# Optimization experiments

Measured on AMD Instinct MI355X. Metric: run time of the kernel, lower is better.

The kernel has to match this reference:

```python
import jax, jax.numpy as jnp
import numpy as np

B, P, H, E, A, V, L = 64, 196, 512, 512, 512, 30000, 21  # batch, pixels, hidden, embed, attn, vocab, cap_len
T = L - 1  # max decode steps


def setup_inputs() -> dict:
    key = jax.random.key(0)
    ks = jax.random.split(key, 16)
    s = 0.02
    lengths = jnp.sort(jax.random.randint(ks[2], (B,), 5, L + 1))[::-1]
    lengths = lengths.at[0].set(L)  # ensure max decode length == T
    return {
        "encoder_out": jax.random.normal(ks[0], (B, P, H), jnp.float32),
        "captions": jax.random.randint(ks[1], (B, L), 0, V),
        "lengths": lengths,
        "emb": jax.random.normal(ks[3], (V, E), jnp.float32) * s,
        "W_ea": jax.random.normal(ks[4], (A, H), jnp.float32) * s,
        "b_ea": jnp.zeros((A,), jnp.float32),
        "W_da": jax.random.normal(ks[5], (A, H), jnp.float32) * s,
        "b_da": jnp.zeros((A,), jnp.float32),
        "W_fa": jax.random.normal(ks[6], (1, A), jnp.float32) * s,
        "b_fa": jnp.zeros((1,), jnp.float32),
        "W_fb": jax.random.normal(ks[7], (H, H), jnp.float32) * s,
        "b_fb": jnp.zeros((H,), jnp.float32),
        "W_ih": jax.random.normal(ks[8], (4 * H, E + H), jnp.float32) * s,
        "W_hh": jax.random.normal(ks[9], (4 * H, H), jnp.float32) * s,
        "b_ih": jnp.zeros((4 * H,), jnp.float32),
        "b_hh": jnp.zeros((4 * H,), jnp.float32),
        "W_fc": jax.random.normal(ks[10], (V, H), jnp.float32) * s,
        "b_fc": jnp.zeros((V,), jnp.float32),
    }


def reference(encoder_out, captions, lengths, emb, W_ea, b_ea, W_da, b_da,
              W_fa, b_fa, W_fb, b_fb, W_ih, W_hh, b_ih, b_hh, W_fc, b_fc):
    # init hidden state = mean over pixels
    h0 = encoder_out.mean(axis=1)  # (B, H)
    c0 = h0
    # precompute encoder attention projection (loop-invariant)
    att1 = jnp.einsum("bph,ah->bpa", encoder_out, W_ea) + b_ea  # (B, P, A)
    emb_seq = emb[captions[:, :T]]  # (B, T, E)
    # active[t, b] = decode_length_b > t  (captions assumed sorted desc by length)
    active = (lengths[None, :] - 1) > jnp.arange(T)[:, None]  # (T, B)

    def step(carry, xs):
        h, c = carry
        emb_t, act = xs  # (B, E), (B,)
        # Bahdanau attention
        att2 = h @ W_da.T + b_da  # (B, A)
        e = (jax.nn.relu(att1 + att2[:, None, :]) @ W_fa.T).squeeze(-1) + b_fa[0]  # (B, P)
        alpha = jax.nn.softmax(e, axis=1)
        awe = jnp.einsum("bph,bp->bh", encoder_out, alpha)  # (B, H)
        gate = jax.nn.sigmoid(h @ W_fb.T + b_fb)
        awe = gate * awe
        x = jnp.concatenate([emb_t, awe], axis=1)  # (B, E+H)
        gates = x @ W_ih.T + b_ih + h @ W_hh.T + b_hh  # (B, 4H)
        i, f, g, o = jnp.split(gates, 4, axis=1)
        c_new = jax.nn.sigmoid(f) * c + jax.nn.sigmoid(i) * jnp.tanh(g)
        h_new = jax.nn.sigmoid(o) * jnp.tanh(c_new)
        preds = h_new @ W_fc.T + b_fc  # (B, V)
        m = act[:, None].astype(h.dtype)
        return (h_new, c_new), (preds * m, alpha * m)

    (_, _), (preds_t, alphas_t) = jax.lax.scan(
        step, (h0, c0), (emb_seq.transpose(1, 0, 2), active))
    predictions = preds_t.transpose(1, 0, 2)  # (B, T, V)
    alphas = alphas_t.transpose(1, 0, 2)      # (B, T, P)
    return predictions, alphas
```

## Files before the change

### kernel.cpp

```cpp
#include <hip/hip_runtime.h>
#include <hip/hip_bf16.h>

typedef _Float16 f16;
typedef __attribute__((ext_vector_type(8))) _Float16 f16x8;
typedef __attribute__((ext_vector_type(2))) _Float16 f16x2;
typedef __attribute__((ext_vector_type(4))) float f32x4;

constexpr int CB = 64, CP = 196, CH = 512, CV = 30000, CVP = 30080, CT = 20;
constexpr int NT = 235;

__device__ __forceinline__ float sigf(float x) { return 1.f / (1.f + __expf(-x)); }

#if defined(__has_builtin)
#if __has_builtin(__builtin_amdgcn_fdot2)
#define HAVE_FDOT2 1
#endif
#endif

__device__ __forceinline__ f16x2 asf16x2(unsigned u) {
    union { unsigned x; f16x2 h; } c; c.x = u; return c.h;
}
__device__ __forceinline__ float dotp(f16x2 a, f16x2 b, float c) {
#ifdef HAVE_FDOT2
    return __builtin_amdgcn_fdot2(a, b, c, false);
#else
    return fmaf((float)a[0], (float)b[0], fmaf((float)a[1], (float)b[1], c));
#endif
}

__device__ __forceinline__ unsigned ald_u(const unsigned* p) {
    return __hip_atomic_load(p, __ATOMIC_RELAXED, __HIP_MEMORY_SCOPE_AGENT);
}
__device__ __forceinline__ void ast_u(unsigned* p, unsigned v) {
    __hip_atomic_store(p, v, __ATOMIC_RELAXED, __HIP_MEMORY_SCOPE_AGENT);
}
__device__ __forceinline__ float ald_f(const float* p) {
    return __hip_atomic_load(p, __ATOMIC_RELAXED, __HIP_MEMORY_SCOPE_AGENT);
}
__device__ __forceinline__ void ast_f(float* p, float v) {
    __hip_atomic_store(p, v, __ATOMIC_RELAXED, __HIP_MEMORY_SCOPE_AGENT);
}

__device__ __forceinline__ void wait4(const int* slotbase, int target) {
    if (threadIdx.x < 64) {
        for (;;) {
            int v = __hip_atomic_load(slotbase + (threadIdx.x & 3), __ATOMIC_RELAXED,
                                      __HIP_MEMORY_SCOPE_AGENT);
            if (__all(v >= target)) break;
            __builtin_amdgcn_s_sleep(1);
        }
    }
    __builtin_amdgcn_s_barrier();
    __builtin_amdgcn_sched_barrier(0);
}
__device__ __forceinline__ void post4(int* slot, int val) {
    __syncthreads();
    if (threadIdx.x == 0)
        __hip_atomic_store(slot, val, __ATOMIC_RELAXED, __HIP_MEMORY_SCOPE_AGENT);
}

__device__ __forceinline__ void cvt8(const float* __restrict__ s, f16* __restrict__ d) {
    float4 a = *(const float4*)s;
    float4 b = *(const float4*)(s + 4);
    f16x8 o;
    o[0] = (f16)a.x; o[1] = (f16)a.y; o[2] = (f16)a.z; o[3] = (f16)a.w;
    o[4] = (f16)b.x; o[5] = (f16)b.y; o[6] = (f16)b.z; o[7] = (f16)b.w;
    *(f16x8*)d = o;
}

__global__ __launch_bounds__(256) void k_mega(
    const float* __restrict__ enc, const float* __restrict__ W_ea,
    const float* __restrict__ W_da, const float* __restrict__ W_fb,
    const float* __restrict__ W_ih, const float* __restrict__ W_hh,
    const float* __restrict__ W_fc, const float* __restrict__ emb,
    const int* __restrict__ caps, const float* __restrict__ b_da,
    const float* __restrict__ b_fb, const float* __restrict__ b_ih,
    const float* __restrict__ b_hh,
    f16* __restrict__ enc_h, f16* __restrict__ Wea_h, f16* __restrict__ W1q4,
    f16* __restrict__ BpQ4, f16* __restrict__ WihE_p, f16* __restrict__ Wfc_h,
    f16* __restrict__ embg, float* __restrict__ bcat, float* __restrict__ bsum_p,
    int* __restrict__ gsync)
{
    constexpr long long E0 = 802816;
    constexpr long long E1 = E0 + 32768;
    constexpr long long E2 = E1 + 1920000;
    constexpr long long E3 = E2 + 5120;
    constexpr long long E4 = E3 + 81920;
    constexpr long long E5 = E4 + 65536;
    constexpr long long E6 = E5 + 262144;
    constexpr long long E7 = E6 + 131072;
    constexpr long long E8 = E7 + 3072;
    constexpr long long TOT = E8 + 4096;

    for (long long id = (long long)blockIdx.x * 256 + threadIdx.x; id < TOT;
         id += (long long)gridDim.x * 256) {
        if (id < E0) {
            cvt8(enc + id * 8, enc_h + id * 8);
        } else if (id < E1) {
            long long c = id - E0; cvt8(W_ea + c * 8, Wea_h + c * 8);
        } else if (id < E2) {
            long long c = id - E1; cvt8(W_fc + c * 8, Wfc_h + c * 8);
        } else if (id < E3) {
            long long c = id - E2; f16x8 z = {};
            *(f16x8*)&Wfc_h[15360000 + c * 8] = z;
        } else if (id < E4) {
            long long c = id - E3; int m = (int)(c >> 6), j = (int)(c & 63);
            int tt = m >> 6, bb = m & 63;
            int row = caps[bb * 21 + tt];
            cvt8(emb + (size_t)row * 512 + j * 8, embg + (size_t)m * 512 + j * 8);
        } else if (id < E5) {
            long long c = id - E4;
            int qq = (int)(c >> 14), kk4 = (int)((c >> 8) & 63), o = (int)(c & 255);
            const float* src = (o < 128) ? &W_da[(size_t)(128 * qq + o) * 512]
                                         : &W_fb[(size_t)(128 * qq + o - 128) * 512];
            cvt8(src + kk4 * 8, &W1q4[(((size_t)qq * 64 + kk4) * 256 + o) * 8]);
        } else if (id < E6) {
            long long c = id - E5;
            int qq = (int)(c >> 16), kk4 = (int)((c >> 9) & 127), o = (int)(c & 511);
            int d = 128 * qq + (o >> 2), g = o & 3;
            int r = g * 512 + d;
            const float* src = (kk4 < 64) ? &W_ih[(size_t)r * 1024 + 512 + kk4 * 8]
                                          : &W_hh[(size_t)r * 512 + kk4 * 8 - 512];
            cvt8(src, &BpQ4[(((size_t)qq * 128 + kk4) * 512 + o) * 8]);
        } else if (id < E7) {
            long long c = id - E6;
            int cc = (int)(c >> 6), j8 = (int)(c & 63);
            int r = (cc & 3) * 512 + (cc >> 2);
            cvt8(W_ih + (size_t)r * 1024 + j8 * 8, WihE_p + (size_t)cc * 512 + j8 * 8);
        } else if (id < E8) {
            int i = (int)(id - E7);
            if (i < 512) bcat[i] = b_da[i];
            else if (i < 1024) bcat[i] = b_fb[i - 512];
            else {
                int cc = i - 1024;
                int r = (cc & 3) * 512 + (cc >> 2);
                bsum_p[cc] = b_ih[r] + b_hh[r];
            }
        } else {
            gsync[(int)(id - E8)] = 0;
        }
    }
}

__global__ __launch_bounds__(256) void k_h0(const float* __restrict__ enc,
                                            f16* __restrict__ hbuf, float* __restrict__ cinit)
{
    int b = blockIdx.x;
    for (int h = threadIdx.x; h < CH; h += 256) {
        const float* p = enc + (size_t)b * CP * CH + h;
        float s = 0.f;
        for (int q = 0; q < CP; ++q) s += p[q * CH];
        s *= (1.f / 196.f);
        hbuf[b * CH + h] = (f16)s;
        cinit[b * CH + h] = s;
    }
}

enum { EPI_F16B = 0, EPI_F32B = 1, EPI_PREDS = 2 };

template <int EPI>
__global__ __launch_bounds__(256) void gemm_k512(
    const f16* __restrict__ Aptr, const f16* __restrict__ Bptr, int N,
    const float* __restrict__ bias, float* __restrict__ Cf,
    f16* __restrict__ Ch, const int* __restrict__ lengths)
{
    constexpr int LD = 40;
    const int tid = threadIdx.x;
    const int lane = tid & 63, wave = tid >> 6;
    const int wr = wave >> 1, wc = wave & 1;
    int bx, by;
    if constexpr (EPI == EPI_PREDS) {
        int bid1 = blockIdx.x;
        int nt = (bid1 / 80) * 8 + (bid1 & 7);
        int mt = (bid1 >> 3) % 10;
        if (nt >= NT) return;
        bx = nt; by = mt;
    } else {
        bx = blockIdx.x; by = blockIdx.y;
    }

    __shared__ f16 As[128 * LD];
    __shared__ f16 Bs[128 * LD];

    const f16* Ag = Aptr + (size_t)by * 128 * 512;
    const f16* Bg = Bptr + (size_t)bx * 128 * 512;

    int srow[2], skc[2];
#pragma unroll
    for (int i = 0; i < 2; ++i) { int ci = tid + i * 256; srow[i] = ci >> 2; skc[i] = (ci & 3) * 8; }

    f32x4 acc[4][4] = {};
    f16x8 ar[2], br[2];
#pragma unroll
    for (int i = 0; i < 2; ++i) {
        ar[i] = *(const f16x8*)&Ag[(size_t)srow[i] * 512 + skc[i]];
        br[i] = *(const f16x8*)&Bg[(size_t)srow[i] * 512 + skc[i]];
    }

    const int rr = lane & 15, kg = (lane >> 4) * 8;
    for (int kt = 0; kt < 16; ++kt) {
        __syncthreads();
#pragma unroll
        for (int i = 0; i < 2; ++i) {
            *(f16x8*)&As[srow[i] * LD + skc[i]] = ar[i];
            *(f16x8*)&Bs[srow[i] * LD + skc[i]] = br[i];
        }
        __syncthreads();
        if (kt < 15) {
            int k0 = (kt + 1) * 32;
#pragma unroll
            for (int i = 0; i < 2; ++i) {
                ar[i] = *(const f16x8*)&Ag[(size_t)srow[i] * 512 + k0 + skc[i]];
                br[i] = *(const f16x8*)&Bg[(size_t)srow[i] * 512 + k0 + skc[i]];
            }
        }
        f16x8 af[4], bf[4];
#pragma unroll
        for (int mi = 0; mi < 4; ++mi) af[mi] = *(const f16x8*)&As[(wr * 64 + mi * 16 + rr) * LD + kg];
#pragma unroll
        for (int ni = 0; ni < 4; ++ni) bf[ni] = *(const f16x8*)&Bs[(wc * 64 + ni * 16 + rr) * LD + kg];
#pragma unroll
        for (int mi = 0; mi < 4; ++mi)
#pragma unroll
            for (int ni = 0; ni < 4; ++ni)
                acc[mi][ni] = __builtin_amdgcn_mfma_f32_16x16x32_f16(af[mi], bf[ni], acc[mi][ni], 0, 0, 0);
    }

    const int m0 = by * 128 + wr * 64;
    const int n0 = bx * 128 + wc * 64;
    const int r0 = (lane >> 4) * 4, cc = lane & 15;
#pragma unroll
    for (int mi = 0; mi < 4; ++mi) {
#pragma unroll
        for (int ni = 0; ni < 4; ++ni) {
#pragma unroll
            for (int r = 0; r < 4; ++r) {
                int m = m0 + mi * 16 + r0 + r;
                int n = n0 + ni * 16 + cc;
                float v = acc[mi][ni][r];
                if constexpr (EPI == EPI_F16B) {
                    Ch[(size_t)m * N + n] = (f16)(v + bias[n]);
                } else if constexpr (EPI == EPI_F32B) {
                    Cf[(size_t)m * N + n] = v + bias[n];
                } else {
                    if (n < CV) {
                        int tt = m >> 6, b = m & 63;
                        float val = ((lengths[b] - 1) > tt) ? (v + bias[n]) : 0.f;
                        __builtin_nontemporal_store(val, &Cf[(size_t)b * (CT * CV) + (size_t)tt * CV + n]);
                    }
                }
            }
        }
    }
}

__global__ __launch_bounds__(512) void k_loop4(
    const f16* __restrict__ att1, const f16* __restrict__ ench,
    const f16* __restrict__ W1q4, const f16* __restrict__ BpQ4,
    const float* __restrict__ embIH, const float* __restrict__ Wfa,
    const float* __restrict__ bfa, const float* __restrict__ bcat,
    const int* __restrict__ lens, const float* __restrict__ cinit,
    f16* __restrict__ hbuf, float* __restrict__ alph,
    float* __restrict__ xatt2, float* __restrict__ xe,
    float* __restrict__ xxa, int* __restrict__ gsync)
{
    const int bid = blockIdx.x, tid = threadIdx.x;
    const int lane = tid & 63, wv = tid >> 6;
    const int b = bid >> 2, q = bid & 3;

    int* s1 = gsync + b * 16;
    int* s2 = gsync + 1024 + b * 16;
    int* s3 = gsync + 2048 + b * 16;
    int* s4 = gsync + 3072 + b * 16;

    __shared__ __align__(16) f16 h_s[512];
    __shared__ float c_s[128];
    __shared__ float a2f[512];
    __shared__ float ga_s[128];
    __shared__ float es[196], als[196], red[16];
    __shared__ float part1[2][256];
    __shared__ float awp[32][128];
    __shared__ __align__(16) f16 xh_s[1024];
    __shared__ float gt[512];
    __shared__ f16 htmp[128];

    if (tid < 256) ((unsigned*)h_s)[tid] = ((const unsigned*)(hbuf + b * 512))[tid];
    if (tid < 128) c_s[tid] = cinit[b * 512 + 128 * q + tid];
    const float bfa0 = bfa[0];
    const int lb = lens[b];
    float wfr[8];
#pragma unroll
    for (int j = 0; j < 8; ++j) wfr[j] = Wfa[lane * 8 + j];
    const int ecnt = (56 - wv) >> 3;
    const int ar_ = lane >> 4, ac_ = lane & 15;
    __syncthreads();

    for (int t = 0; t < CT; ++t) {
        if (t > 0) {
            wait4(s4, t);
            if (tid < 256)
                ((unsigned*)h_s)[tid] =
                    ald_u((const unsigned*)(hbuf + (size_t)t * 32768 + b * 512) + tid);
            __syncthreads();
        }

        {
            const int kh = tid >> 8, oo = tid & 255;
            const f16* wp = W1q4 + (((size_t)q * 64 + kh * 32) * 256 + oo) * 8;
            const uint4* xq = (const uint4*)h_s + kh * 32;
            float a0 = 0.f, a1 = 0.f, a2 = 0.f, a3 = 0.f;
#pragma unroll 8
            for (int i = 0; i < 32; ++i) {
                uint4 w = *(const uint4*)(wp + (size_t)i * 2048);
                uint4 xv = xq[i];
                a0 = dotp(asf16x2(w.x), asf16x2(xv.x), a0);
                a1 = dotp(asf16x2(w.y), asf16x2(xv.y), a1);
                a2 = dotp(asf16x2(w.z), asf16x2(xv.z), a2);
                a3 = dotp(asf16x2(w.w), asf16x2(xv.w), a3);
            }
            part1[kh][oo] = (a0 + a1) + (a2 + a3);
        }
        __syncthreads();
        if (tid < 256) {
            float v = part1[0][tid] + part1[1][tid];
            if (tid < 128) {
                v += bcat[128 * q + tid];
                ast_f(&xatt2[b * 512 + 128 * q + tid], v);
            } else {
                ga_s[tid - 128] = v + bcat[512 + 128 * q + (tid - 128)];
            }
        }

        f16x8 fr[7];
#pragma unroll
        for (int i = 0; i < 7; ++i)
            if (i < ecnt)
                fr[i] = *(const f16x8*)&att1[((size_t)b * CP + 49 * q + wv + 8 * i) * 512 + lane * 8];

        post4(s1 + q, t + 1);
        wait4(s1, t + 1);
        a2f[tid] = ald_f(&xatt2[b * 512 + tid]);
        __syncthreads();

        {
            float a2r[8];
#pragma unroll
            for (int j = 0; j < 8; ++j) a2r[j] = a2f[lane * 8 + j];
#pragma unroll
            for (int i = 0; i < 7; ++i)
                if (i < ecnt) {
                    float e = 0.f;
#pragma unroll
                    for (int j = 0; j < 8; ++j)
                        e += fmaxf((float)fr[i][j] + a2r[j], 0.f) * wfr[j];
#pragma unroll
                    for (int o = 32; o; o >>= 1) e += __shfl_down(e, o);
                    if (lane == 0) ast_f(&xe[b * 196 + 49 * q + wv + 8 * i], e + bfa0);
                }
        }

        f16x8 er[7];
#pragma unroll
        for (int it = 0; it < 7; ++it) {
            int p = it * 32 + wv * 4 + ar_;
            if (p < CP)
                er[it] = *(const f16x8*)&ench[((size_t)b * CP + p) * 512 + 128 * q + ac_ * 8];
        }

        post4(s2 + q, t + 1);
        wait4(s2, t + 1);
        if (tid < CP) es[tid] = ald_f(&xe[b * 196 + tid]);
        __syncthreads();

        {
            float ev = (tid < CP) ? es[tid] : -1e30f;
            float mx = ev;
#pragma unroll
            for (int o = 32; o; o >>= 1) mx = fmaxf(mx, __shfl_down(mx, o));
            if (lane == 0) red[wv] = mx;
            __syncthreads();
            mx = red[0];
#pragma unroll
            for (int w = 1; w < 8; ++w) mx = fmaxf(mx, red[w]);
            float ex = (tid < CP) ? __expf(ev - mx) : 0.f;
            float sm = ex;
#pragma unroll
            for (int o = 32; o; o >>= 1) sm += __shfl_down(sm, o);
            if (lane == 0) red[8 + wv] = sm;
            __syncthreads();
            sm = red[8];
#pragma unroll
            for (int w = 1; w < 8; ++w) sm += red[8 + w];
            float al = ex / sm;
            if (tid < CP) {
                als[tid] = al;
                if (tid >= 49 * q && tid < 49 * (q + 1))
                    alph[(size_t)b * (CT * CP) + t * CP + tid] = ((lb - 1) > t) ? al : 0.f;
            }
        }
        __syncthreads();
        {
            float aw[8] = {};
#pragma unroll
            for (int it = 0; it < 7; ++it) {
                int p = it * 32 + wv * 4 + ar_;
                if (p < CP) {
                    float a = als[p];
#pragma unroll
                    for (int j = 0; j < 8; ++j) aw[j] = fmaf(a, (float)er[it][j], aw[j]);
                }
            }
#pragma unroll
            for (int j = 0; j < 8; ++j) awp[wv * 4 + ar_][ac_ * 8 + j] = aw[j];
        }
        __syncthreads();
        if (tid < 128) {
            float s = 0.f;
#pragma unroll
            for (int g = 0; g < 32; ++g) s += awp[g][tid];
            ast_f(&xxa[b * 512 + 128 * q + tid], sigf(ga_s[tid]) * s);
        }
        post4(s3 + q, t + 1);
        wait4(s3, t + 1);
        xh_s[tid] = (f16)ald_f(&xxa[b * 512 + tid]);
        xh_s[512 + tid] = h_s[tid];
        __syncthreads();

        {
            const f16* wp = BpQ4 + ((size_t)q * 128 * 512 + tid) * 8;
            const uint4* xq = (const uint4*)xh_s;
            float a0 = 0.f, a1 = 0.f, a2 = 0.f, a3 = 0.f;
#pragma unroll 8
            for (int i = 0; i < 128; ++i) {
                uint4 w = *(const uint4*)(wp + (size_t)i * 4096);
                uint4 xv = xq[i];
                a0 = dotp(asf16x2(w.x), asf16x2(xv.x), a0);
                a1 = dotp(asf16x2(w.y), asf16x2(xv.y), a1);
                a2 = dotp(asf16x2(w.z), asf16x2(xv.z), a2);
                a3 = dotp(asf16x2(w.w), asf16x2(xv.w), a3);
            }
            gt[tid] = (a0 + a1) + (a2 + a3)
                      + embIH[(size_t)(t * 64 + b) * 2048 + 512 * q + tid];
        }
        __syncthreads();
        if (tid < 128) {
            float gi = gt[4 * tid], gf = gt[4 * tid + 1];
            float gg = gt[4 * tid + 2], go = gt[4 * tid + 3];
            float cn = sigf(gf) * c_s[tid] + sigf(gi) * tanhf(gg);
            c_s[tid] = cn;
            htmp[tid] = (f16)(sigf(go) * tanhf(cn));
        }
        __syncthreads();
        if (tid < 64) {
            union { f16 h[2]; unsigned u; } pk;
            pk.h[0] = htmp[2 * tid]; pk.h[1] = htmp[2 * tid + 1];
            ast_u((unsigned*)&hbuf[(size_t)(t + 1) * 32768 + b * 512 + 128 * q] + tid, pk.u);
        }
        post4(s4 + q, t + 1);
    }
}

extern "C" void kernel_launch(void* const* d_in, const int* in_sizes, int n_in,
                              void* d_out, int out_size, void* d_ws, size_t ws_size,
                              hipStream_t stream)
{
    const float* enc  = (const float*)d_in[0];
    const int*   caps = (const int*)d_in[1];
    const int*   lens = (const int*)d_in[2];
    const float* emb  = (const float*)d_in[3];
    const float* W_ea = (const float*)d_in[4];
    const float* b_ea = (const float*)d_in[5];
    const float* W_da = (const float*)d_in[6];
    const float* b_da = (const float*)d_in[7];
    const float* W_fa = (const float*)d_in[8];
    const float* b_fa = (const float*)d_in[9];
    const float* W_fb = (const float*)d_in[10];
    const float* b_fb = (const float*)d_in[11];
    const float* W_ih = (const float*)d_in[12];
    const float* W_hh = (const float*)d_in[13];
    const float* b_ih = (const float*)d_in[14];
    const float* b_hh = (const float*)d_in[15];
    const float* W_fc = (const float*)d_in[16];
    const float* b_fc = (const float*)d_in[17];

    float* out = (float*)d_out;
    float* alph_out = out + (size_t)CB * CT * CV;

    char* p = (char*)d_ws;
    auto carve = [&](size_t bytes) {
        char* r = p;
        p += (bytes + 255) & ~(size_t)255;
        return r;
    };
    f16* enc_h   = (f16*)carve((size_t)12544 * 512 * 2);
    f16* att1_h  = (f16*)carve((size_t)12544 * 512 * 2);
    f16* Wea_h   = (f16*)carve((size_t)512 * 512 * 2);
    f16* W1q4    = (f16*)carve((size_t)4 * 64 * 256 * 8 * 2);
    f16* BpQ4    = (f16*)carve((size_t)4 * 128 * 512 * 8 * 2);
    f16* WihE_p  = (f16*)carve((size_t)2048 * 512 * 2);
    f16* Wfc_h   = (f16*)carve((size_t)CVP * 512 * 2);
    f16* embg    = (f16*)carve((size_t)1280 * 512 * 2);
    float* embIH = (float*)carve((size_t)1280 * 2048 * 4);
    float* bcat  = (float*)carve(1024 * 4);
    float* bsum_p= (float*)carve(2048 * 4);
    f16* hbuf    = (f16*)carve((size_t)21 * 64 * 512 * 2);
    float* cinit = (float*)carve((size_t)64 * 512 * 4);
    float* xatt2 = (float*)carve((size_t)64 * 512 * 4);
    float* xe    = (float*)carve((size_t)64 * 196 * 4);
    float* xxa   = (float*)carve((size_t)64 * 512 * 4);
    int* gsync   = (int*)carve(4096 * 4);

    hipLaunchKernelGGL(k_mega, dim3(4096), dim3(256), 0, stream,
                       enc, W_ea, W_da, W_fb, W_ih, W_hh, W_fc, emb, caps,
                       b_da, b_fb, b_ih, b_hh,
                       enc_h, Wea_h, W1q4, BpQ4, WihE_p, Wfc_h, embg, bcat, bsum_p, gsync);

    hipLaunchKernelGGL(k_h0, dim3(64), dim3(256), 0, stream, enc, hbuf, cinit);

    hipLaunchKernelGGL((gemm_k512<EPI_F16B>), dim3(4, 98), dim3(256), 0, stream,
                       enc_h, Wea_h, 512, b_ea, (float*)nullptr, att1_h, (const int*)nullptr);
    hipLaunchKernelGGL((gemm_k512<EPI_F32B>), dim3(16, 10), dim3(256), 0, stream,
                       embg, WihE_p, 2048, bsum_p, embIH, (f16*)nullptr, (const int*)nullptr);

    hipLaunchKernelGGL(k_loop4, dim3(256), dim3(512), 0, stream,
                       att1_h, enc_h, W1q4, BpQ4, embIH, W_fa, b_fa, bcat,
                       lens, cinit, hbuf, alph_out, xatt2, xe, xxa, gsync);

    hipLaunchKernelGGL((gemm_k512<EPI_PREDS>), dim3(2400), dim3(256), 0, stream,
                       hbuf + 32768, Wfc_h, CVP, b_fc, out, (f16*)nullptr, lens);
}
```

Before: 553.8 us.

## Regroup recurrent loop blocks so each weight slice serves four batch rows

The persistent decode loop is repartitioned from 4 blocks per batch row to groups of 16 blocks sharing 4 batch rows. Each block now owns a slice of the output features for the W_da/W_fb and LSTM gate matvecs and applies it to all 4 rows at once. This cuts the per-step weight traffic from L2 by reusing each loaded weight element across four hidden vectors. In exchange, sync barriers now span 16 blocks instead of 4, and the h/gate data must be exchanged across the wider group through global memory.

New measurement: 546.1 us. Within noise of the previous version (-1.4%).

```diff
diff --git a/kernel.cpp b/kernel.cpp
--- a/kernel.cpp
+++ b/kernel.cpp
@@ -41,10 +41,10 @@
     __hip_atomic_store(p, v, __ATOMIC_RELAXED, __HIP_MEMORY_SCOPE_AGENT);
 }
 
-__device__ __forceinline__ void wait4(const int* slotbase, int target) {
+__device__ __forceinline__ void wait16(const int* base, int target) {
     if (threadIdx.x < 64) {
         for (;;) {
-            int v = __hip_atomic_load(slotbase + (threadIdx.x & 3), __ATOMIC_RELAXED,
+            int v = __hip_atomic_load(base + (threadIdx.x & 15), __ATOMIC_RELAXED,
                                       __HIP_MEMORY_SCOPE_AGENT);
             if (__all(v >= target)) break;
             __builtin_amdgcn_s_sleep(1);
@@ -53,7 +53,7 @@
     __builtin_amdgcn_s_barrier();
     __builtin_amdgcn_sched_barrier(0);
 }
-__device__ __forceinline__ void post4(int* slot, int val) {
+__device__ __forceinline__ void post16(int* slot, int val) {
     __syncthreads();
     if (threadIdx.x == 0)
         __hip_atomic_store(slot, val, __ATOMIC_RELAXED, __HIP_MEMORY_SCOPE_AGENT);
@@ -76,8 +76,8 @@
     const int* __restrict__ caps, const float* __restrict__ b_da,
     const float* __restrict__ b_fb, const float* __restrict__ b_ih,
     const float* __restrict__ b_hh,
-    f16* __restrict__ enc_h, f16* __restrict__ Wea_h, f16* __restrict__ W1q4,
-    f16* __restrict__ BpQ4, f16* __restrict__ WihE_p, f16* __restrict__ Wfc_h,
+    f16* __restrict__ enc_h, f16* __restrict__ Wea_h, f16* __restrict__ W1L,
+    f16* __restrict__ BpL, f16* __restrict__ WihE_p, f16* __restrict__ Wfc_h,
     f16* __restrict__ embg, float* __restrict__ bcat, float* __restrict__ bsum_p,
     int* __restrict__ gsync)
 {
@@ -90,7 +90,7 @@
     constexpr long long E6 = E5 + 262144;
     constexpr long long E7 = E6 + 131072;
     constexpr long long E8 = E7 + 3072;
-    constexpr long long TOT = E8 + 4096;
+    constexpr long long TOT = E8 + 1024;
 
     for (long long id = (long long)blockIdx.x * 256 + threadIdx.x; id < TOT;
          id += (long long)gridDim.x * 256) {
@@ -110,18 +110,19 @@
             cvt8(emb + (size_t)row * 512 + j * 8, embg + (size_t)m * 512 + j * 8);
         } else if (id < E5) {
             long long c = id - E4;
-            int qq = (int)(c >> 14), kk4 = (int)((c >> 8) & 63), o = (int)(c & 255);
-            const float* src = (o < 128) ? &W_da[(size_t)(128 * qq + o) * 512]
-                                         : &W_fb[(size_t)(128 * qq + o - 128) * 512];
-            cvt8(src + kk4 * 8, &W1q4[(((size_t)qq * 64 + kk4) * 256 + o) * 8]);
+            int o = (int)(c & 63), kk4 = (int)((c >> 6) & 63), s = (int)(c >> 12);
+            int O = 64 * s + o;
+            const float* src = (O < 512) ? &W_da[(size_t)O * 512]
+                                         : &W_fb[(size_t)(O - 512) * 512];
+            cvt8(src + kk4 * 8, &W1L[(((size_t)s * 64 + kk4) * 64 + o) * 8]);
         } else if (id < E6) {
             long long c = id - E5;
-            int qq = (int)(c >> 16), kk4 = (int)((c >> 9) & 127), o = (int)(c & 511);
-            int d = 128 * qq + (o >> 2), g = o & 3;
+            int o = (int)(c & 127), kk4 = (int)((c >> 7) & 127), s = (int)(c >> 14);
+            int d = 32 * s + (o >> 2), g = o & 3;
             int r = g * 512 + d;
             const float* src = (kk4 < 64) ? &W_ih[(size_t)r * 1024 + 512 + kk4 * 8]
-                                          : &W_hh[(size_t)r * 512 + kk4 * 8 - 512];
-            cvt8(src, &BpQ4[(((size_t)qq * 128 + kk4) * 512 + o) * 8]);
+                                          : &W_hh[(size_t)r * 512 + (kk4 - 64) * 8];
+            cvt8(src, &BpL[(((size_t)s * 128 + kk4) * 128 + o) * 8]);
         } else if (id < E7) {
             long long c = id - E6;
             int cc = (int)(c >> 6), j8 = (int)(c & 63);
@@ -254,9 +255,9 @@
     }
 }
 
-__global__ __launch_bounds__(512) void k_loop4(
+__global__ __launch_bounds__(512) void k_loopQ(
     const f16* __restrict__ att1, const f16* __restrict__ ench,
-    const f16* __restrict__ W1q4, const f16* __restrict__ BpQ4,
+    const f16* __restrict__ W1L, const f16* __restrict__ BpL,
     const float* __restrict__ embIH, const float* __restrict__ Wfa,
     const float* __restrict__ bfa, const float* __restrict__ bcat,
     const int* __restrict__ lens, const float* __restrict__ cinit,
@@ -266,80 +267,95 @@
 {
     const int bid = blockIdx.x, tid = threadIdx.x;
     const int lane = tid & 63, wv = tid >> 6;
-    const int b = bid >> 2, q = bid & 3;
-
-    int* s1 = gsync + b * 16;
-    int* s2 = gsync + 1024 + b * 16;
-    int* s3 = gsync + 2048 + b * 16;
-    int* s4 = gsync + 3072 + b * 16;
-
-    __shared__ __align__(16) f16 h_s[512];
-    __shared__ float c_s[128];
-    __shared__ float a2f[512];
-    __shared__ float ga_s[128];
+    const int q4 = bid >> 4, s = bid & 15;
+    const int b0 = 4 * q4;
+    const int batt = b0 + (s & 3), q = s >> 2;
+
+    int* sl = gsync + q4 * 64;
+
+    __shared__ __align__(16) f16 h_s[4 * 512];
+    __shared__ __align__(16) float part[2048];
+    __shared__ float a2f[512], ga_s[128];
     __shared__ float es[196], als[196], red[16];
-    __shared__ float part1[2][256];
     __shared__ float awp[32][128];
-    __shared__ __align__(16) f16 xh_s[1024];
+    __shared__ __align__(16) f16 xh_s[4 * 1024];
     __shared__ float gt[512];
     __shared__ f16 htmp[128];
-
-    if (tid < 256) ((unsigned*)h_s)[tid] = ((const unsigned*)(hbuf + b * 512))[tid];
-    if (tid < 128) c_s[tid] = cinit[b * 512 + 128 * q + tid];
+    __shared__ float c_s[128];
+
+    ((unsigned*)h_s)[tid] = ((const unsigned*)(hbuf + b0 * 512))[tid];
+    ((unsigned*)h_s)[tid + 512] = ((const unsigned*)(hbuf + b0 * 512))[tid + 512];
+    if (tid < 128) c_s[tid] = cinit[(b0 + (tid >> 5)) * 512 + 32 * s + (tid & 31)];
+
     const float bfa0 = bfa[0];
-    const int lb = lens[b];
+    const int lb = lens[batt];
     float wfr[8];
 #pragma unroll
     for (int j = 0; j < 8; ++j) wfr[j] = Wfa[lane * 8 + j];
     const int ecnt = (56 - wv) >> 3;
     const int ar_ = lane >> 4, ac_ = lane & 15;
+    const int ks1 = tid >> 6, o1 = tid & 63;
+    const int ks4 = tid >> 7, o4 = tid & 127;
     __syncthreads();
 
     for (int t = 0; t < CT; ++t) {
         if (t > 0) {
-            wait4(s4, t);
-            if (tid < 256)
-                ((unsigned*)h_s)[tid] =
-                    ald_u((const unsigned*)(hbuf + (size_t)t * 32768 + b * 512) + tid);
+            wait16(sl + 48, t);
+            const unsigned* hp = (const unsigned*)(hbuf + (size_t)t * 32768 + b0 * 512);
+            ((unsigned*)h_s)[tid] = ald_u(hp + tid);
+            ((unsigned*)h_s)[tid + 512] = ald_u(hp + tid + 512);
             __syncthreads();
         }
 
         {
-            const int kh = tid >> 8, oo = tid & 255;
-            const f16* wp = W1q4 + (((size_t)q * 64 + kh * 32) * 256 + oo) * 8;
-            const uint4* xq = (const uint4*)h_s + kh * 32;
+            const f16* wp = W1L + (((size_t)s * 64 + ks1 * 8) * 64 + o1) * 8;
+            const uint4* xq = (const uint4*)h_s;
             float a0 = 0.f, a1 = 0.f, a2 = 0.f, a3 = 0.f;
-#pragma unroll 8
-            for (int i = 0; i < 32; ++i) {
-                uint4 w = *(const uint4*)(wp + (size_t)i * 2048);
-                uint4 xv = xq[i];
-                a0 = dotp(asf16x2(w.x), asf16x2(xv.x), a0);
-                a1 = dotp(asf16x2(w.y), asf16x2(xv.y), a1);
-                a2 = dotp(asf16x2(w.z), asf16x2(xv.z), a2);
-                a3 = dotp(asf16x2(w.w), asf16x2(xv.w), a3);
-            }
-            part1[kh][oo] = (a0 + a1) + (a2 + a3);
+#pragma unroll 4
+            for (int i = 0; i < 8; ++i) {
+                uint4 w = *(const uint4*)(wp + (size_t)i * 512);
+                int kk4 = ks1 * 8 + i;
+                uint4 x0 = xq[kk4], x1 = xq[64 + kk4], x2 = xq[128 + kk4], x3 = xq[192 + kk4];
+                a0 = dotp(asf16x2(w.x), asf16x2(x0.x), a0);
+                a1 = dotp(asf16x2(w.x), asf16x2(x1.x), a1);
+                a2 = dotp(asf16x2(w.x), asf16x2(x2.x), a2);
+                a3 = dotp(asf16x2(w.x), asf16x2(x3.x), a3);
+                a0 = dotp(asf16x2(w.y), asf16x2(x0.y), a0);
+                a1 = dotp(asf16x2(w.y), asf16x2(x1.y), a1);
+                a2 = dotp(asf16x2(w.y), asf16x2(x2.y), a2);
+                a3 = dotp(asf16x2(w.y), asf16x2(x3.y), a3);
+                a0 = dotp(asf16x2(w.z), asf16x2(x0.z), a0);
+                a1 = dotp(asf16x2(w.z), asf16x2(x1.z), a1);
+                a2 = dotp(asf16x2(w.z), asf16x2(x2.z), a2);
+                a3 = dotp(asf16x2(w.z), asf16x2(x3.z), a3);
+                a0 = dotp(asf16x2(w.w), asf16x2(x0.w), a0);
+                a1 = dotp(asf16x2(w.w), asf16x2(x1.w), a1);
+                a2 = dotp(asf16x2(w.w), asf16x2(x2.w), a2);
+                a3 = dotp(asf16x2(w.w), asf16x2(x3.w), a3);
+            }
+            f32x4 pk; pk[0] = a0; pk[1] = a1; pk[2] = a2; pk[3] = a3;
+            *(f32x4*)&part[ks1 * 256 + o1 * 4] = pk;
         }
         __syncthreads();
         if (tid < 256) {
-            float v = part1[0][tid] + part1[1][tid];
-            if (tid < 128) {
-                v += bcat[128 * q + tid];
-                ast_f(&xatt2[b * 512 + 128 * q + tid], v);
-            } else {
-                ga_s[tid - 128] = v + bcat[512 + 128 * q + (tid - 128)];
-            }
+            float v = 0.f;
+#pragma unroll
+            for (int w8 = 0; w8 < 8; ++w8) v += part[w8 * 256 + tid];
+            int o = tid >> 2, bb = tid & 3;
+            int O = 64 * s + o;
+            ast_f(&xatt2[(size_t)(b0 + bb) * 1024 + O], v + bcat[O]);
         }
 
         f16x8 fr[7];
 #pragma unroll
         for (int i = 0; i < 7; ++i)
             if (i < ecnt)
-                fr[i] = *(const f16x8*)&att1[((size_t)b * CP + 49 * q + wv + 8 * i) * 512 + lane * 8];
-
-        post4(s1 + q, t + 1);
-        wait4(s1, t + 1);
-        a2f[tid] = ald_f(&xatt2[b * 512 + tid]);
+                fr[i] = *(const f16x8*)&att1[((size_t)batt * CP + 49 * q + wv + 8 * i) * 512 + lane * 8];
+
+        post16(sl + s, t + 1);
+        wait16(sl, t + 1);
+        a2f[tid] = ald_f(&xatt2[(size_t)batt * 1024 + tid]);
+        if (tid < 128) ga_s[tid] = ald_f(&xatt2[(size_t)batt * 1024 + 512 + 128 * q + tid]);
         __syncthreads();
 
         {
@@ -355,7 +371,7 @@
                         e += fmaxf((float)fr[i][j] + a2r[j], 0.f) * wfr[j];
 #pragma unroll
                     for (int o = 32; o; o >>= 1) e += __shfl_down(e, o);
-                    if (lane == 0) ast_f(&xe[b * 196 + 49 * q + wv + 8 * i], e + bfa0);
+                    if (lane == 0) ast_f(&xe[batt * 196 + 49 * q + wv + 8 * i], e + bfa0);
                 }
         }
 
@@ -364,12 +380,12 @@
         for (int it = 0; it < 7; ++it) {
             int p = it * 32 + wv * 4 + ar_;
             if (p < CP)
-                er[it] = *(const f16x8*)&ench[((size_t)b * CP + p) * 512 + 128 * q + ac_ * 8];
-        }
-
-        post4(s2 + q, t + 1);
-        wait4(s2, t + 1);
-        if (tid < CP) es[tid] = ald_f(&xe[b * 196 + tid]);
+                er[it] = *(const f16x8*)&ench[((size_t)batt * CP + p) * 512 + 128 * q + ac_ * 8];
+        }
+
+        post16(sl + 16 + s, t + 1);
+        wait16(sl + 16, t + 1);
+        if (tid < CP) es[tid] = ald_f(&xe[batt * 196 + tid]);
         __syncthreads();
 
         {
@@ -395,7 +411,7 @@
             if (tid < CP) {
                 als[tid] = al;
                 if (tid >= 49 * q && tid < 49 * (q + 1))
-                    alph[(size_t)b * (CT * CP) + t * CP + tid] = ((lb - 1) > t) ? al : 0.f;
+                    alph[(size_t)batt * (CT * CP) + t * CP + tid] = ((lb - 1) > t) ? al : 0.f;
             }
         }
         __syncthreads();
@@ -415,48 +431,82 @@
         }
         __syncthreads();
         if (tid < 128) {
-            float s = 0.f;
-#pragma unroll
-            for (int g = 0; g < 32; ++g) s += awp[g][tid];
-            ast_f(&xxa[b * 512 + 128 * q + tid], sigf(ga_s[tid]) * s);
-        }
-        post4(s3 + q, t + 1);
-        wait4(s3, t + 1);
-        xh_s[tid] = (f16)ald_f(&xxa[b * 512 + tid]);
-        xh_s[512 + tid] = h_s[tid];
+            float sv = 0.f;
+#pragma unroll
+            for (int g = 0; g < 32; ++g) sv += awp[g][tid];
+            ast_f(&xxa[batt * 512 + 128 * q + tid], sigf(ga_s[tid]) * sv);
+        }
+        post16(sl + 32 + s, t + 1);
+        wait16(sl + 32, t + 1);
+#pragma unroll
+        for (int k = 0; k < 4; ++k) {
+            int c4 = k * 512 + tid;
+            int bb = c4 >> 9, j = c4 & 511;
+            xh_s[bb * 1024 + j] = (f16)ald_f(&xxa[(b0 + bb) * 512 + j]);
+        }
+#pragma unroll
+        for (int k = 0; k < 2; ++k) {
+            int u = k * 512 + tid;
+            int bb = u >> 8, jj = u & 255;
+            ((unsigned*)xh_s)[bb * 512 + 256 + jj] = ((unsigned*)h_s)[bb * 256 + jj];
+        }
         __syncthreads();
 
         {
-            const f16* wp = BpQ4 + ((size_t)q * 128 * 512 + tid) * 8;
+            const f16* wp = BpL + (((size_t)s * 128 + ks4 * 32) * 128 + o4) * 8;
             const uint4* xq = (const uint4*)xh_s;
             float a0 = 0.f, a1 = 0.f, a2 = 0.f, a3 = 0.f;
-#pragma unroll 8
-            for (int i = 0; i < 128; ++i) {
-                uint4 w = *(const uint4*)(wp + (size_t)i * 4096);
-                uint4 xv = xq[i];
-                a0 = dotp(asf16x2(w.x), asf16x2(xv.x), a0);
-                a1 = dotp(asf16x2(w.y), asf16x2(xv.y), a1);
-                a2 = dotp(asf16x2(w.z), asf16x2(xv.z), a2);
-                a3 = dotp(asf16x2(w.w), asf16x2(xv.w), a3);
-            }
-            gt[tid] = (a0 + a1) + (a2 + a3)
-                      + embIH[(size_t)(t * 64 + b) * 2048 + 512 * q + tid];
+#pragma unroll 4
+            for (int i = 0; i < 32; ++i) {
+                uint4 w = *(const uint4*)(wp + (size_t)i * 1024);
+                int kk4 = ks4 * 32 + i;
+                uint4 x0 = xq[kk4], x1 = xq[128 + kk4], x2 = xq[256 + kk4], x3 = xq[384 + kk4];
+                a0 = dotp(asf16x2(w.x), asf16x2(x0.x), a0);
+                a1 = dotp(asf16x2(w.x), asf16x2(x1.x), a1);
+                a2 = dotp(asf16x2(w.x), asf16x2(x2.x), a2);
+                a3 = dotp(asf16x2(w.x), asf16x2(x3.x), a3);
+                a0 = dotp(asf16x2(w.y), asf16x2(x0.y), a0);
+                a1 = dotp(asf16x2(w.y), asf16x2(x1.y), a1);
+                a2 = dotp(asf16x2(w.y), asf16x2(x2.y), a2);
+                a3 = dotp(asf16x2(w.y), asf16x2(x3.y), a3);
+                a0 = dotp(asf16x2(w.z), asf16x2(x0.z), a0);
+                a1 = dotp(asf16x2(w.z), asf16x2(x1.z), a1);
+                a2 = dotp(asf16x2(w.z), asf16x2(x2.z), a2);
+                a3 = dotp(asf16x2(w.z), asf16x2(x3.z), a3);
+                a0 = dotp(asf16x2(w.w), asf16x2(x0.w), a0);
+                a1 = dotp(asf16x2(w.w), asf16x2(x1.w), a1);
+                a2 = dotp(asf16x2(w.w), asf16x2(x2.w), a2);
+                a3 = dotp(asf16x2(w.w), asf16x2(x3.w), a3);
+            }
+            f32x4 pk; pk[0] = a0; pk[1] = a1; pk[2] = a2; pk[3] = a3;
+            *(f32x4*)&part[ks4 * 512 + o4 * 4] = pk;
+        }
+        __syncthreads();
+        {
+            float g = part[tid] + part[512 + tid] + part[1024 + tid] + part[1536 + tid];
+            int o = tid >> 2, bb = tid & 3;
+            gt[tid] = g + embIH[(size_t)(t * 64 + b0 + bb) * 2048 + 128 * s + o];
         }
         __syncthreads();
         if (tid < 128) {
-            float gi = gt[4 * tid], gf = gt[4 * tid + 1];
-            float gg = gt[4 * tid + 2], go = gt[4 * tid + 3];
-            float cn = sigf(gf) * c_s[tid] + sigf(gi) * tanhf(gg);
-            c_s[tid] = cn;
-            htmp[tid] = (f16)(sigf(go) * tanhf(cn));
+            int dd = tid >> 2, bb = tid & 3;
+            float gi = gt[(4 * dd + 0) * 4 + bb];
+            float gf = gt[(4 * dd + 1) * 4 + bb];
+            float gg = gt[(4 * dd + 2) * 4 + bb];
+            float go = gt[(4 * dd + 3) * 4 + bb];
+            float cn = sigf(gf) * c_s[bb * 32 + dd] + sigf(gi) * tanhf(gg);
+            c_s[bb * 32 + dd] = cn;
+            htmp[bb * 32 + dd] = (f16)(sigf(go) * tanhf(cn));
         }
         __syncthreads();
         if (tid < 64) {
+            int bb = tid >> 4, dd2 = (tid & 15) * 2;
             union { f16 h[2]; unsigned u; } pk;
-            pk.h[0] = htmp[2 * tid]; pk.h[1] = htmp[2 * tid + 1];
-            ast_u((unsigned*)&hbuf[(size_t)(t + 1) * 32768 + b * 512 + 128 * q] + tid, pk.u);
-        }
-        post4(s4 + q, t + 1);
+            pk.h[0] = htmp[bb * 32 + dd2]; pk.h[1] = htmp[bb * 32 + dd2 + 1];
+            size_t off = (size_t)(t + 1) * 32768 + (b0 + bb) * 512 + 32 * s + dd2;
+            ast_u((unsigned*)hbuf + (off >> 1), pk.u);
+        }
+        post16(sl + 48 + s, t + 1);
     }
 }
 
@@ -495,8 +545,8 @@
     f16* enc_h   = (f16*)carve((size_t)12544 * 512 * 2);
     f16* att1_h  = (f16*)carve((size_t)12544 * 512 * 2);
     f16* Wea_h   = (f16*)carve((size_t)512 * 512 * 2);
-    f16* W1q4    = (f16*)carve((size_t)4 * 64 * 256 * 8 * 2);
-    f16* BpQ4    = (f16*)carve((size_t)4 * 128 * 512 * 8 * 2);
+    f16* W1L     = (f16*)carve((size_t)16 * 64 * 64 * 8 * 2);
+    f16* BpL     = (f16*)carve((size_t)16 * 128 * 128 * 8 * 2);
     f16* WihE_p  = (f16*)carve((size_t)2048 * 512 * 2);
     f16* Wfc_h   = (f16*)carve((size_t)CVP * 512 * 2);
     f16* embg    = (f16*)carve((size_t)1280 * 512 * 2);
@@ -505,15 +555,15 @@
     float* bsum_p= (float*)carve(2048 * 4);
     f16* hbuf    = (f16*)carve((size_t)21 * 64 * 512 * 2);
     float* cinit = (float*)carve((size_t)64 * 512 * 4);
-    float* xatt2 = (float*)carve((size_t)64 * 512 * 4);
+    float* xatt2 = (float*)carve((size_t)64 * 1024 * 4);
     float* xe    = (float*)carve((size_t)64 * 196 * 4);
     float* xxa   = (float*)carve((size_t)64 * 512 * 4);
-    int* gsync   = (int*)carve(4096 * 4);
+    int* gsync   = (int*)carve(1024 * 4);
 
     hipLaunchKernelGGL(k_mega, dim3(4096), dim3(256), 0, stream,
                        enc, W_ea, W_da, W_fb, W_ih, W_hh, W_fc, emb, caps,
                        b_da, b_fb, b_ih, b_hh,
-                       enc_h, Wea_h, W1q4, BpQ4, WihE_p, Wfc_h, embg, bcat, bsum_p, gsync);
+                       enc_h, Wea_h, W1L, BpL, WihE_p, Wfc_h, embg, bcat, bsum_p, gsync);
 
     hipLaunchKernelGGL(k_h0, dim3(64), dim3(256), 0, stream, enc, hbuf, cinit);
 
@@ -522,8 +572,8 @@
     hipLaunchKernelGGL((gemm_k512<EPI_F32B>), dim3(16, 10), dim3(256), 0, stream,
                        embg, WihE_p, 2048, bsum_p, embIH, (f16*)nullptr, (const int*)nullptr);
 
-    hipLaunchKernelGGL(k_loop4, dim3(256), dim3(512), 0, stream,
-                       att1_h, enc_h, W1q4, BpQ4, embIH, W_fa, b_fa, bcat,
+    hipLaunchKernelGGL(k_loopQ, dim3(256), dim3(512), 0, stream,
+                       att1_h, enc_h, W1L, BpL, embIH, W_fa, b_fa, bcat,
                        lens, cinit, hbuf, alph_out, xatt2, xe, xxa, gsync);
 
     hipLaunchKernelGGL((gemm_k512<EPI_PREDS>), dim3(2400), dim3(256), 0, stream,
```
